# Performance work log

Hardware: AMD Instinct MI355X
Metric: run time of the kernel (lower is better)

## Reference

```python
import jax, jax.numpy as jnp
import numpy as np

# pywt Wavelet('db4') decomposition filters (dec_lo, dec_hi), 8 taps
DEC_LO = jnp.array([-0.010597401784997278, 0.032883011666982945, 0.030841381835986965,
                    -0.18703481171888114, -0.02798376941698385, 0.6308807679295904,
                    0.7148465705525415, 0.23037781330885523], dtype=jnp.float32)
DEC_HI = jnp.array([-0.23037781330885523, 0.7148465705525415, -0.6308807679295904,
                    -0.02798376941698385, 0.18703481171888114, 0.030841381835986965,
                    -0.032883011666982945, -0.010597401784997278], dtype=jnp.float32)
FILT_LEN = 8
LEVEL = 3


def _dwt_step(a):
    """Single-level DWT matching pywt.dwt(a, 'db4', mode='symmetric') along last axis.

    pywt equivalence: np.convolve(np.pad(x, L-1, 'symmetric'), f, 'valid')[1::2].
    np.convolve flips the filter, so we cross-correlate with the reversed filter,
    starting at offset 1 with stride 2.
    a: [B, N] -> (cA, cD) each [B, floor((N + L - 1)/2)]
    """
    p = FILT_LEN - 1
    xp = jnp.pad(a, ((0, 0), (p, p)), mode='symmetric')[:, 1:]  # [B, N+2p-1]
    k = jnp.stack([DEC_LO[::-1], DEC_HI[::-1]])[:, None, :]      # [2, 1, L] (OIH)
    y = jax.lax.conv_general_dilated(
        xp[:, None, :].astype(a.dtype), k.astype(a.dtype),
        window_strides=(2,), padding='VALID',
        dimension_numbers=('NCH', 'OIH', 'NCH'))                 # [B, 2, M]
    return y[:, 0, :], y[:, 1, :]


def wavedec_features(x):
    """pywt.wavedec(x, 'db4', level=3) -> concat of flattened [cA3, cD3, cD2, cD1]."""
    a = x
    details = []
    for _ in range(LEVEL):
        a, d = _dwt_step(a)
        details.append(d)
    coeffs = [a] + details[::-1]
    return jnp.concatenate([c.reshape(-1) for c in coeffs])


def setup_inputs() -> dict:
    key = jax.random.key(0)
    x = jax.random.normal(key, (4096, 8192), dtype=jnp.float32)
    return {"x": x}


def reference(x):
    return wavedec_features(x)
```

## Files before the change

kernel.cpp:

```cpp
#include <hip/hip_runtime.h>


constexpr int N0 = 8192;
constexpr int M1 = 4099;
constexpr int M2 = 2053;
constexpr int M3 = 1030;
constexpr int NT = 256;

typedef float vfloat4 __attribute__((ext_vector_type(4)));

__device__ __forceinline__ int symidx(int o, int n) {
    if (o < 0) o = -1 - o;
    if (o >= n) o = 2 * n - 1 - o;
    return o;
}

__device__ __forceinline__ void compute4(const float* __restrict__ w,
                                         float* __restrict__ a,
                                         float* __restrict__ d) {
    constexpr float RLO[8] = {0.23037781330885523f,  0.7148465705525415f,
                              0.6308807679295904f,   -0.02798376941698385f,
                              -0.18703481171888114f, 0.030841381835986965f,
                              0.032883011666982945f, -0.010597401784997278f};
    constexpr float RHI[8] = {-0.010597401784997278f, -0.032883011666982945f,
                              0.030841381835986965f,  0.18703481171888114f,
                              -0.02798376941698385f,  -0.6308807679295904f,
                              0.7148465705525415f,    -0.23037781330885523f};
#pragma unroll
    for (int j = 0; j < 4; ++j) {
        float aj = 0.f, dj = 0.f;
#pragma unroll
        for (int t = 0; t < 8; ++t) {
            const float v = w[2 * j + 2 + t];
            aj = fmaf(RLO[t], v, aj);
            dj = fmaf(RHI[t], v, dj);
        }
        a[j] = aj;
        d[j] = dj;
    }
}

template <int PAD>
__device__ __forceinline__ void chunk(const float* __restrict__ in, int i0,
                                      float* __restrict__ a,
                                      float* __restrict__ d) {
    float w[16 + (PAD ? 4 : 0)];
    const float4* p = reinterpret_cast<const float4*>(in + 2 * i0 - 8 - PAD);
    *reinterpret_cast<float4*>(&w[0]) = p[0];
    *reinterpret_cast<float4*>(&w[4]) = p[1];
    *reinterpret_cast<float4*>(&w[8]) = p[2];
    *reinterpret_cast<float4*>(&w[12]) = p[3];
    if constexpr (PAD != 0) *reinterpret_cast<float4*>(&w[16]) = p[4];
    compute4(w + PAD, a, d);
}

__device__ __forceinline__ void edge_pair(const float* in, int n, int i,
                                          float& a, float& d) {
    constexpr float LO[8] = {
        -0.010597401784997278f, 0.032883011666982945f, 0.030841381835986965f,
        -0.18703481171888114f,  -0.02798376941698385f, 0.6308807679295904f,
        0.7148465705525415f,    0.23037781330885523f};
    constexpr float HI[8] = {
        -0.23037781330885523f,  0.7148465705525415f,   -0.6308807679295904f,
        -0.02798376941698385f,  0.18703481171888114f,  0.030841381835986965f,
        -0.032883011666982945f, -0.010597401784997278f};
    a = 0.f;
    d = 0.f;
#pragma unroll
    for (int s = 0; s < 8; ++s) {
        const float v = in[symidx(2 * i + 1 - s, n)];
        a = fmaf(LO[s], v, a);
        d = fmaf(HI[s], v, d);
    }
}

__device__ __forceinline__ void ntst4(float* dst, float a0, float a1, float a2,
                                      float a3) {
    vfloat4 v = {a0, a1, a2, a3};
    __builtin_nontemporal_store(v, reinterpret_cast<vfloat4*>(dst));
}

__global__ __launch_bounds__(NT) void WaveletFeatures_77214922047612_kernel(
    const float* __restrict__ x, float* __restrict__ out, int B) {
    __shared__ __align__(16) float s1[M1 + 8];
    __shared__ __align__(16) float s2[M2 + 8];

    const int row = blockIdx.x;
    const int tid = threadIdx.x;
    const int r4 = row & 3;
    const float* xr = x + (size_t)row * N0;

    float* ca3 = out + (size_t)row * M3;
    float* cd3 = out + (size_t)B * M3 + (size_t)row * M3;
    float* cd2 = out + 2 * (size_t)B * M3 + (size_t)row * M2;
    float* cd1 = out + (size_t)B * (2 * M3 + M2) + (size_t)row * M1;

    {
        const int ph = r4;
        const int lo = ph + 4;
        const int cap = (ph & 1) ? 4091 : 4092;
        const int C = (cap - lo) / 4 + 1;
        const int hi = lo + 4 * C;
        if (ph & 1) {
            for (int c = tid; c < C; c += NT) {
                const int i0 = lo + 4 * c;
                float a[4], d[4];
                chunk<2>(xr, i0, a, d);
                s1[i0] = a[0]; s1[i0 + 1] = a[1]; s1[i0 + 2] = a[2]; s1[i0 + 3] = a[3];
                ntst4(&cd1[i0], d[0], d[1], d[2], d[3]);
            }
        } else {
            for (int c = tid; c < C; c += NT) {
                const int i0 = lo + 4 * c;
                float a[4], d[4];
                chunk<0>(xr, i0, a, d);
                s1[i0] = a[0]; s1[i0 + 1] = a[1]; s1[i0 + 2] = a[2]; s1[i0 + 3] = a[3];
                ntst4(&cd1[i0], d[0], d[1], d[2], d[3]);
            }
        }
        const int nl = lo, nr = M1 - hi;
        if (tid < nl + nr) {
            const int i = tid < nl ? tid : hi + (tid - nl);
            float a, d;
            edge_pair(xr, N0, i, a, d);
            s1[i] = a;
            cd1[i] = d;
        }
    }
    __syncthreads();

    {
        const int ph = (4 - r4) & 3;
        const int lo = ph + 4;
        const int cap = 2045;
        const int C = (cap - lo) / 4 + 1;
        const int hi = lo + 4 * C;
        if (ph & 1) {
            for (int c = tid; c < C; c += NT) {
                const int i0 = lo + 4 * c;
                float a[4], d[4];
                chunk<2>(s1, i0, a, d);
                s2[i0] = a[0]; s2[i0 + 1] = a[1]; s2[i0 + 2] = a[2]; s2[i0 + 3] = a[3];
                ntst4(&cd2[i0], d[0], d[1], d[2], d[3]);
            }
        } else {
            for (int c = tid; c < C; c += NT) {
                const int i0 = lo + 4 * c;
                float a[4], d[4];
                chunk<0>(s1, i0, a, d);
                s2[i0] = a[0]; s2[i0 + 1] = a[1]; s2[i0 + 2] = a[2]; s2[i0 + 3] = a[3];
                ntst4(&cd2[i0], d[0], d[1], d[2], d[3]);
            }
        }
        const int nl = lo, nr = M2 - hi;
        if (tid < nl + nr) {
            const int i = tid < nl ? tid : hi + (tid - nl);
            float a, d;
            edge_pair(s1, M1, i, a, d);
            s2[i] = a;
            cd2[i] = d;
        }
    }
    __syncthreads();

    {
        const int ph = (2 * r4) & 3;
        const int lo = ph + 4;
        const int cap = 1022;
        const int C = (cap - lo) / 4 + 1;
        const int hi = lo + 4 * C;
        for (int c = tid; c < C; c += NT) {
            const int i0 = lo + 4 * c;
            float a[4], d[4];
            chunk<0>(s2, i0, a, d);
            ntst4(&ca3[i0], a[0], a[1], a[2], a[3]);
            ntst4(&cd3[i0], d[0], d[1], d[2], d[3]);
        }
        const int nl = lo, nr = M3 - hi;
        if (tid < nl + nr) {
            const int i = tid < nl ? tid : hi + (tid - nl);
            float a, d;
            edge_pair(s2, M2, i, a, d);
            ca3[i] = a;
            cd3[i] = d;
        }
    }
}

extern "C" void kernel_launch(void* const* d_in, const int* in_sizes, int n_in,
                              void* d_out, int out_size, void* d_ws,
                              size_t ws_size, hipStream_t stream) {
    const float* x = (const float*)d_in[0];
    float* out = (float*)d_out;
    const int B = in_sizes[0] / N0;
    WaveletFeatures_77214922047612_kernel<<<dim3(B), dim3(NT), 0, stream>>>(
        x, out, B);
}
```

Baseline: 47.19 us.

## Split each row across two blocks with halo recompute and stage input in LDS

Each row is now handled by two blocks, each covering half the signal plus an overlapping halo, so the grid doubles to 2*B blocks. Each block first copies its input segment into shared memory and then runs all three DWT levels from LDS. Halo coefficients are recomputed redundantly, and only owned outputs are written. The aim is more parallelism and shorter per-block serial chains. The cost is extra redundant halo work, a larger shared footprint that may cut occupancy, and an added load-and-sync stage.

```diff
diff --git a/kernel.cpp b/kernel.cpp
--- a/kernel.cpp
+++ b/kernel.cpp
@@ -45,12 +45,15 @@
                                       float* __restrict__ a,
                                       float* __restrict__ d) {
     float w[16 + (PAD ? 4 : 0)];
-    const float4* p = reinterpret_cast<const float4*>(in + 2 * i0 - 8 - PAD);
-    *reinterpret_cast<float4*>(&w[0]) = p[0];
-    *reinterpret_cast<float4*>(&w[4]) = p[1];
-    *reinterpret_cast<float4*>(&w[8]) = p[2];
-    *reinterpret_cast<float4*>(&w[12]) = p[3];
-    if constexpr (PAD != 0) *reinterpret_cast<float4*>(&w[16]) = p[4];
+    const float* p = in + 2 * i0 - 8 - PAD;
+    *reinterpret_cast<float4*>(&w[0]) = *reinterpret_cast<const float4*>(p);
+    *reinterpret_cast<float4*>(&w[4]) = *reinterpret_cast<const float4*>(p + 4);
+    *reinterpret_cast<float4*>(&w[8]) = *reinterpret_cast<const float4*>(p + 8);
+    *reinterpret_cast<float4*>(&w[12]) =
+        *reinterpret_cast<const float4*>(p + 12);
+    if constexpr (PAD != 0)
+        *reinterpret_cast<float4*>(&w[16]) =
+            *reinterpret_cast<const float4*>(p + 16);
     compute4(w + PAD, a, d);
 }
 
@@ -74,18 +77,20 @@
     }
 }
 
-__device__ __forceinline__ void ntst4(float* dst, float a0, float a1, float a2,
-                                      float a3) {
-    vfloat4 v = {a0, a1, a2, a3};
-    __builtin_nontemporal_store(v, reinterpret_cast<vfloat4*>(dst));
+__device__ __forceinline__ void ntst4(float* dst, const float* v) {
+    vfloat4 t = {v[0], v[1], v[2], v[3]};
+    __builtin_nontemporal_store(t, reinterpret_cast<vfloat4*>(dst));
 }
 
 __global__ __launch_bounds__(NT) void WaveletFeatures_77214922047612_kernel(
     const float* __restrict__ x, float* __restrict__ out, int B) {
-    __shared__ __align__(16) float s1[M1 + 8];
-    __shared__ __align__(16) float s2[M2 + 8];
-
-    const int row = blockIdx.x;
+    __shared__ __align__(16) float sx[4132];
+    __shared__ __align__(16) float s1[2068];
+    __shared__ __align__(16) float s2[1036];
+
+    const int bid = blockIdx.x;
+    const int row = bid >> 1;
+    const int seg = bid & 1;
     const int tid = threadIdx.x;
     const int r4 = row & 3;
     const float* xr = x + (size_t)row * N0;
@@ -95,92 +100,131 @@
     float* cd2 = out + 2 * (size_t)B * M3 + (size_t)row * M2;
     float* cd1 = out + (size_t)B * (2 * M3 + M2) + (size_t)row * M1;
 
-    {
-        const int ph = r4;
-        const int lo = ph + 4;
-        const int cap = (ph & 1) ? 4091 : 4092;
-        const int C = (cap - lo) / 4 + 1;
-        const int hi = lo + 4 * C;
-        if (ph & 1) {
-            for (int c = tid; c < C; c += NT) {
-                const int i0 = lo + 4 * c;
-                float a[4], d[4];
-                chunk<2>(xr, i0, a, d);
-                s1[i0] = a[0]; s1[i0 + 1] = a[1]; s1[i0 + 2] = a[2]; s1[i0 + 3] = a[3];
-                ntst4(&cd1[i0], d[0], d[1], d[2], d[3]);
-            }
-        } else {
-            for (int c = tid; c < C; c += NT) {
-                const int i0 = lo + 4 * c;
-                float a[4], d[4];
-                chunk<0>(xr, i0, a, d);
-                s1[i0] = a[0]; s1[i0 + 1] = a[1]; s1[i0 + 2] = a[2]; s1[i0 + 3] = a[3];
-                ntst4(&cd1[i0], d[0], d[1], d[2], d[3]);
-            }
-        }
-        const int nl = lo, nr = M1 - hi;
+    const int ph1 = r4;
+    const int ph2 = (4 - r4) & 3;
+    const int ph3 = (2 * r4) & 3;
+
+    const int xlo = seg ? 4084 : 0;
+    float* const sxg = sx - xlo;
+    float* const s1g = s1 - (seg ? 2044 : 0);
+    float* const s2g = s2 - (seg ? 1024 : 0);
+
+    {
+        const int nx4 = seg ? 1027 : 1032;
+        const float4* src = reinterpret_cast<const float4*>(xr + xlo);
+        float4* dst = reinterpret_cast<float4*>(sx);
+        for (int k = tid; k < nx4; k += NT) dst[k] = src[k];
+    }
+    __syncthreads();
+
+    {
+        int clo, chi, sl0, sr1, own0, own1;
+        if (seg) {
+            clo = 2052 + ph1;
+            chi = (ph1 == 0) ? 4092 : (ph1 == 1) ? 4089 : (ph1 == 2) ? 4090 : 4091;
+            sl0 = 2046; sr1 = 4099; own0 = 2052; own1 = 4099;
+        } else {
+            clo = ph1 + 4;
+            chi = (ph1 == 0) ? 2048 : 2044 + ph1;
+            sl0 = 0; sr1 = 2064; own0 = 0; own1 = 2052;
+        }
+        const int C = (chi - clo) / 4 + 1;
+        if (ph1 & 1) {
+            for (int c = tid; c < C; c += NT) {
+                const int i0 = clo + 4 * c;
+                float a[4], d[4];
+                chunk<2>(sxg, i0, a, d);
+                s1g[i0] = a[0]; s1g[i0 + 1] = a[1];
+                s1g[i0 + 2] = a[2]; s1g[i0 + 3] = a[3];
+                ntst4(&cd1[i0], d);
+            }
+        } else {
+            for (int c = tid; c < C; c += NT) {
+                const int i0 = clo + 4 * c;
+                float a[4], d[4];
+                chunk<0>(sxg, i0, a, d);
+                s1g[i0] = a[0]; s1g[i0 + 1] = a[1];
+                s1g[i0 + 2] = a[2]; s1g[i0 + 3] = a[3];
+                ntst4(&cd1[i0], d);
+            }
+        }
+        const int nl = clo - sl0, nr = sr1 - (chi + 4);
         if (tid < nl + nr) {
-            const int i = tid < nl ? tid : hi + (tid - nl);
+            const int i = tid < nl ? sl0 + tid : chi + 4 + (tid - nl);
             float a, d;
-            edge_pair(xr, N0, i, a, d);
-            s1[i] = a;
-            cd1[i] = d;
+            edge_pair(sxg, N0, i, a, d);
+            s1g[i] = a;
+            if (i >= own0 && i < own1) cd1[i] = d;
         }
     }
     __syncthreads();
 
     {
-        const int ph = (4 - r4) & 3;
-        const int lo = ph + 4;
-        const int cap = 2045;
-        const int C = (cap - lo) / 4 + 1;
-        const int hi = lo + 4 * C;
-        if (ph & 1) {
-            for (int c = tid; c < C; c += NT) {
-                const int i0 = lo + 4 * c;
-                float a[4], d[4];
-                chunk<2>(s1, i0, a, d);
-                s2[i0] = a[0]; s2[i0 + 1] = a[1]; s2[i0 + 2] = a[2]; s2[i0 + 3] = a[3];
-                ntst4(&cd2[i0], d[0], d[1], d[2], d[3]);
-            }
-        } else {
-            for (int c = tid; c < C; c += NT) {
-                const int i0 = lo + 4 * c;
-                float a[4], d[4];
-                chunk<0>(s1, i0, a, d);
-                s2[i0] = a[0]; s2[i0 + 1] = a[1]; s2[i0 + 2] = a[2]; s2[i0 + 3] = a[3];
-                ntst4(&cd2[i0], d[0], d[1], d[2], d[3]);
-            }
-        }
-        const int nl = lo, nr = M2 - hi;
+        int clo, chi, sl0, sr1, own0, own1;
+        if (seg) {
+            clo = 1028 + ph2;
+            chi = (ph2 == 0) ? 2044 : 2040 + ph2;
+            sl0 = 1026; sr1 = 2053; own0 = 1028; own1 = 2053;
+        } else {
+            clo = ph2 + 4;
+            chi = (ph2 == 0) ? 1024 : 1020 + ph2;
+            sl0 = 0; sr1 = 1032; own0 = 0; own1 = 1028;
+        }
+        const int C = (chi - clo) / 4 + 1;
+        if (ph2 & 1) {
+            for (int c = tid; c < C; c += NT) {
+                const int i0 = clo + 4 * c;
+                float a[4], d[4];
+                chunk<2>(s1g, i0, a, d);
+                s2g[i0] = a[0]; s2g[i0 + 1] = a[1];
+                s2g[i0 + 2] = a[2]; s2g[i0 + 3] = a[3];
+                ntst4(&cd2[i0], d);
+            }
+        } else {
+            for (int c = tid; c < C; c += NT) {
+                const int i0 = clo + 4 * c;
+                float a[4], d[4];
+                chunk<0>(s1g, i0, a, d);
+                s2g[i0] = a[0]; s2g[i0 + 1] = a[1];
+                s2g[i0 + 2] = a[2]; s2g[i0 + 3] = a[3];
+                ntst4(&cd2[i0], d);
+            }
+        }
+        const int nl = clo - sl0, nr = sr1 - (chi + 4);
         if (tid < nl + nr) {
-            const int i = tid < nl ? tid : hi + (tid - nl);
+            const int i = tid < nl ? sl0 + tid : chi + 4 + (tid - nl);
             float a, d;
-            edge_pair(s1, M1, i, a, d);
-            s2[i] = a;
-            cd2[i] = d;
+            edge_pair(s1g, M1, i, a, d);
+            s2g[i] = a;
+            if (i >= own0 && i < own1) cd2[i] = d;
         }
     }
     __syncthreads();
 
     {
-        const int ph = (2 * r4) & 3;
-        const int lo = ph + 4;
-        const int cap = 1022;
-        const int C = (cap - lo) / 4 + 1;
-        const int hi = lo + 4 * C;
+        int clo, chi, sl0, sr1;
+        if (seg) {
+            clo = 516 + ph3;
+            chi = (ph3 == 0) ? 1020 : 1018;
+            sl0 = 516; sr1 = 1030;
+        } else {
+            clo = ph3 + 4;
+            chi = (ph3 == 0) ? 512 : 510;
+            sl0 = 0; sr1 = 516;
+        }
+        const int C = (chi - clo) / 4 + 1;
         for (int c = tid; c < C; c += NT) {
-            const int i0 = lo + 4 * c;
+            const int i0 = clo + 4 * c;
             float a[4], d[4];
-            chunk<0>(s2, i0, a, d);
-            ntst4(&ca3[i0], a[0], a[1], a[2], a[3]);
-            ntst4(&cd3[i0], d[0], d[1], d[2], d[3]);
-        }
-        const int nl = lo, nr = M3 - hi;
+            chunk<0>(s2g, i0, a, d);
+            ntst4(&ca3[i0], a);
+            ntst4(&cd3[i0], d);
+        }
+        const int nl = clo - sl0, nr = sr1 - (chi + 4);
         if (tid < nl + nr) {
-            const int i = tid < nl ? tid : hi + (tid - nl);
+            const int i = tid < nl ? sl0 + tid : chi + 4 + (tid - nl);
             float a, d;
-            edge_pair(s2, M2, i, a, d);
+            edge_pair(s2g, M2, i, a, d);
             ca3[i] = a;
             cd3[i] = d;
         }
@@ -193,6 +237,6 @@
     const float* x = (const float*)d_in[0];
     float* out = (float*)d_out;
     const int B = in_sizes[0] / N0;
-    WaveletFeatures_77214922047612_kernel<<<dim3(B), dim3(NT), 0, stream>>>(
+    WaveletFeatures_77214922047612_kernel<<<dim3(2 * B), dim3(NT), 0, stream>>>(
         x, out, B);
 }
```

New measurement: 55.59 us. +17.8%, slower.
